# Optimization experiments

Measured on AMD Instinct MI355X. Metric: run time of the kernel, lower is better.

Reference implementation:

```python
import jax, jax.numpy as jnp
import numpy as np
from jax import lax

B, S, D, H, K, FF = 8, 1024, 512, 8, 3, 1024
BUCKETS, MAX_REL = 32, 128
DH = D // H
SPAN = BUCKETS  # att_span when position_buckets > 0


def setup_inputs() -> dict:
    key = jax.random.key(0)
    ks = jax.random.split(key, 12)
    n = lambda k, shp, s=0.02: jax.random.normal(k, shp, jnp.float32) * s
    return dict(
        x=jax.random.normal(ks[0], (B, S, D), jnp.float32),
        ln1_g=jnp.ones((D,), jnp.float32), ln1_b=jnp.zeros((D,), jnp.float32),
        dw_w=n(ks[1], (D, 1, K), 0.1), dw_b=jnp.zeros((D,), jnp.float32),
        pw_w=n(ks[2], (D, D)), pw_b=jnp.zeros((D,), jnp.float32),
        ln2_g=jnp.ones((D,), jnp.float32), ln2_b=jnp.zeros((D,), jnp.float32),
        q_w=n(ks[3], (D, D)), q_b=jnp.zeros((D,), jnp.float32),
        k_w=n(ks[4], (D, D)), k_b=jnp.zeros((D,), jnp.float32),
        v_w=n(ks[5], (D, D)), v_b=jnp.zeros((D,), jnp.float32),
        o_w=n(ks[6], (D, D)), o_b=jnp.zeros((D,), jnp.float32),
        rel_emb=n(ks[7], (2 * SPAN, D)),
        ln3_g=jnp.ones((D,), jnp.float32), ln3_b=jnp.zeros((D,), jnp.float32),
        w1=n(ks[8], (FF, D)), b1=jnp.zeros((FF,), jnp.float32),
        w2=n(ks[9], (D, FF)), b2=jnp.zeros((D,), jnp.float32),
    )


def _ln(x, g, b):
    m = x.mean(-1, keepdims=True)
    v = jnp.var(x, axis=-1, keepdims=True)
    return (x - m) * lax.rsqrt(v + 1e-5) * g + b


def _rel_bucket():
    # DeBERTa-v2 log-bucket relative positions, [S, S] int32
    ids = jnp.arange(S, dtype=jnp.int32)
    rel = ids[:, None] - ids[None, :]
    mid = BUCKETS // 2
    sign = jnp.sign(rel)
    abs_pos = jnp.where((rel < mid) & (rel > -mid), mid - 1, jnp.abs(rel)).astype(jnp.float32)
    log_pos = jnp.ceil(jnp.log(abs_pos / mid) / np.log((MAX_REL - 1) / mid) * (mid - 1)) + mid
    return jnp.where(abs_pos <= mid, rel, (log_pos * sign).astype(jnp.int32)).astype(jnp.int32)


def _attention(x, q_w, q_b, k_w, k_b, v_w, v_b, o_w, o_b, rel_emb):
    def heads(t):  # [B,S,D] -> [B,H,S,DH]
        return t.reshape(B, S, H, DH).transpose(0, 2, 1, 3)

    q = heads(x @ q_w.T + q_b)
    k = heads(x @ k_w.T + k_b)
    v = heads(x @ v_w.T + v_b)
    scale = 1.0 / np.sqrt(DH * 3)  # scale_factor = 1 + len(['c2p','p2c'])

    scores = jnp.einsum('bhid,bhjd->bhij', q, k) * scale  # content-to-content

    rel = _rel_bucket()  # [S,S]
    # shared att key: project rel embeddings with same q/k projections -> [H, 2*SPAN, DH]
    pos_k = (rel_emb @ k_w.T + k_b).reshape(2 * SPAN, H, DH).transpose(1, 0, 2)
    pos_q = (rel_emb @ q_w.T + q_b).reshape(2 * SPAN, H, DH).transpose(1, 0, 2)

    # content-to-position
    c2p = jnp.einsum('bhid,hjd->bhij', q, pos_k)  # [B,H,S,2*SPAN]
    c2p_idx = jnp.clip(rel + SPAN, 0, 2 * SPAN - 1)[None, None]  # [1,1,S,S]
    scores = scores + jnp.take_along_axis(c2p, c2p_idx, axis=-1) * scale

    # position-to-content
    p2c = jnp.einsum('bhid,hjd->bhij', k, pos_q)  # [B,H,S,2*SPAN]
    p2c_idx = jnp.clip(-rel + SPAN, 0, 2 * SPAN - 1)[None, None]
    scores = scores + jnp.take_along_axis(p2c, p2c_idx, axis=-1).swapaxes(-1, -2) * scale

    probs = jax.nn.softmax(scores, axis=-1)
    ctx = jnp.einsum('bhij,bhjd->bhid', probs, v).transpose(0, 2, 1, 3).reshape(B, S, D)
    return ctx @ o_w.T + o_b


def reference(x, ln1_g, ln1_b, dw_w, dw_b, pw_w, pw_b, ln2_g, ln2_b,
              q_w, q_b, k_w, k_b, v_w, v_b, o_w, o_b, rel_emb,
              ln3_g, ln3_b, w1, b1, w2, b2):
    # conv block (pre-norm)
    res = x
    xn = _ln(x, ln1_g, ln1_b)
    xc = xn.transpose(0, 2, 1)  # [B,D,S]
    dw = lax.conv_general_dilated(xc, dw_w, (1,), [(K // 2, K // 2)],
                                  dimension_numbers=('NCH', 'OIH', 'NCH'),
                                  feature_group_count=D) + dw_b[None, :, None]
    pw = jnp.einsum('od,bds->bos', pw_w, jax.nn.silu(dw)) + pw_b[None, :, None]
    x = res + pw.transpose(0, 2, 1)
    # attention block
    res = x
    x = res + _attention(_ln(x, ln2_g, ln2_b), q_w, q_b, k_w, k_b, v_w, v_b, o_w, o_b, rel_emb)
    # FFN block
    res = x
    xn = _ln(x, ln3_g, ln3_b)
    ff = jax.nn.silu(xn @ w1.T + b1) @ w2.T + b2
    return res + ff
```

## Files before the change

### kernel.cpp

```cpp
#include <hip/hip_runtime.h>
#include <hip/hip_bf16.h>
#include <math.h>


#define B_  8
#define S_  1024
#define D_  512
#define H_  8
#define DH_ 64
#define FF_ 1024
#define BS_ (B_*S_)
#define SCALE_ 0.07216878364f

typedef __attribute__((ext_vector_type(8))) short  short8;
typedef __attribute__((ext_vector_type(4))) short  short4v;
typedef __attribute__((ext_vector_type(4))) float  f32x4;
typedef __attribute__((ext_vector_type(4))) int    int4v;

static __device__ __forceinline__ float b2f(short u){
  union { int i; float f; } cv; cv.i = ((int)(unsigned short)u) << 16; return cv.f;
}
static __device__ __forceinline__ short f2b(float f){
  union { float f; unsigned u; } cv; cv.f = f;
  unsigned r = cv.u + 0x7FFFu + ((cv.u >> 16) & 1u);
  return (short)(r >> 16);
}
static __device__ __forceinline__ float silu_f(float x){
  return x / (1.f + __expf(-x));
}
static __device__ __forceinline__ f32x4 mfma16(short8 a, short8 b, f32x4 c){
  return __builtin_amdgcn_mfma_f32_16x16x32_bf16(a, b, c, 0, 0, 0);
}
static __device__ __forceinline__ void gl16(const void* g, void* l){
  __builtin_amdgcn_global_load_lds((const __attribute__((address_space(1))) void*)g,
                                   (__attribute__((address_space(3))) void*)l, 16, 0, 0);
}

struct F2B8 { const float* s[8]; short* d[8]; int n[8]; };
__global__ __launch_bounds__(256) void f2b8_kernel(F2B8 a){
  int seg = blockIdx.y;
  int i = (blockIdx.x*256 + threadIdx.x)*4;
  if (i >= a.n[seg]) return;
  float4 v = *(const float4*)(a.s[seg] + i);
  short4v o; o.x = f2b(v.x); o.y = f2b(v.y); o.z = f2b(v.z); o.w = f2b(v.w);
  *(short4v*)(a.d[seg] + i) = o;
}

__global__ __launch_bounds__(256) void tab_kernel(signed char* __restrict__ tab){
  int t = blockIdx.x*256 + threadIdx.x;
  if (t >= 2048) return;
  int d = t - 1023;
  int ad = d < 0 ? -d : d;
  int bkt;
  if (ad <= 16) bkt = d;
  else {
    const float inv_log = 15.f / logf(7.9375f);
    float lp = ceilf(logf((float)ad * (1.f/16.f)) * inv_log) + 16.f;
    int ilp = (int)lp;
    bkt = (d > 0) ? ilp : -ilp;
  }
  int idx = bkt + 32;
  idx = idx < 0 ? 0 : (idx > 63 ? 63 : idx);
  tab[t] = (signed char)idx;
}

__global__ __launch_bounds__(128) void ln_kernel(const float* __restrict__ x,
                                                 const float* __restrict__ g,
                                                 const float* __restrict__ bb,
                                                 short* __restrict__ out){
  int row = blockIdx.x;
  int tid = threadIdx.x;
  float4 v = ((const float4*)(x + (size_t)row*D_))[tid];
  float s  = v.x + v.y + v.z + v.w;
  float ss = v.x*v.x + v.y*v.y + v.z*v.z + v.w*v.w;
  #pragma unroll
  for (int off = 32; off; off >>= 1){ s += __shfl_down(s, off); ss += __shfl_down(ss, off); }
  __shared__ float red[4];
  if ((tid & 63) == 0){ red[tid>>6] = s; red[2 + (tid>>6)] = ss; }
  __syncthreads();
  float S  = red[0] + red[1];
  float SS = red[2] + red[3];
  float m   = S * (1.f/D_);
  float var = SS * (1.f/D_) - m*m;
  float rs  = rsqrtf(var + 1e-5f);
  float4 gv = ((const float4*)g)[tid];
  float4 bv = ((const float4*)bb)[tid];
  short4v o;
  o.x = f2b((v.x - m)*rs*gv.x + bv.x);
  o.y = f2b((v.y - m)*rs*gv.y + bv.y);
  o.z = f2b((v.z - m)*rs*gv.z + bv.z);
  o.w = f2b((v.w - m)*rs*gv.w + bv.w);
  *(short4v*)(out + (size_t)row*D_ + tid*4) = o;
}

__global__ __launch_bounds__(256) void dwconv_kernel(const short* __restrict__ xn,
                                                     const float* __restrict__ w,
                                                     const float* __restrict__ bias,
                                                     short* __restrict__ out){
  int idx = blockIdx.x*256 + threadIdx.x;
  int bs  = idx >> 6;
  int d8  = (idx & 63) << 3;
  int s   = bs & (S_-1);
  const short* base = xn + (size_t)bs*D_ + d8;
  short8 z = {};
  short8 xm = (s > 0)     ? *(const short8*)(base - D_) : z;
  short8 xc =               *(const short8*)(base);
  short8 xp = (s < S_-1)  ? *(const short8*)(base + D_) : z;
  short8 o;
  #pragma unroll
  for (int i = 0; i < 8; i++){
    int d = d8 + i;
    float acc = bias[d] + b2f(xm[i])*w[d*3+0] + b2f(xc[i])*w[d*3+1] + b2f(xp[i])*w[d*3+2];
    o[i] = f2b(silu_f(acc));
  }
  *(short8*)(out + (size_t)bs*D_ + d8) = o;
}

#define GEMM_GL_CORE(AP, WP, KK)                                               \
  __shared__ short a_lds[2][128*64];                                           \
  __shared__ short b_lds[2][64*64];                                            \
  int tid = threadIdx.x;                                                       \
  int w = tid >> 6, lane = tid & 63, quad = lane >> 4, l16 = lane & 15;        \
  int wm = (w >> 1) * 64, wn = (w & 1) * 32;                                   \
  int m0 = blockIdx.x * 128, n0 = blockIdx.y * 64;                             \
  int lr = lane >> 3, lc8 = ((lane & 7) ^ lr) * 8;                             \
  const short* asrc[4]; const short* bsrc[2];                                  \
  _Pragma("unroll")                                                            \
  for (int i = 0; i < 4; i++)                                                  \
    asrc[i] = AP + (size_t)(m0 + w*32 + i*8 + lr)*KK + lc8;                    \
  _Pragma("unroll")                                                            \
  for (int i = 0; i < 2; i++)                                                  \
    bsrc[i] = WP + (size_t)(n0 + w*16 + i*8 + lr)*KK + lc8;                    \
  f32x4 acc[4][2] = {};                                                        \
  int sx = l16 & 7;                                                            \
  _Pragma("unroll")                                                            \
  for (int i = 0; i < 4; i++) gl16(asrc[i], &a_lds[0][(w*32 + i*8)*64]);       \
  _Pragma("unroll")                                                            \
  for (int i = 0; i < 2; i++) gl16(bsrc[i], &b_lds[0][(w*16 + i*8)*64]);       \
  int cur = 0;                                                                 \
  for (int kk = 0; kk < KK; kk += 64){                                         \
    __syncthreads();                                                           \
    if (kk + 64 < KK){                                                         \
      _Pragma("unroll")                                                        \
      for (int i = 0; i < 4; i++)                                              \
        gl16(asrc[i] + kk + 64, &a_lds[cur^1][(w*32 + i*8)*64]);               \
      _Pragma("unroll")                                                        \
      for (int i = 0; i < 2; i++)                                              \
        gl16(bsrc[i] + kk + 64, &b_lds[cur^1][(w*16 + i*8)*64]);               \
    }                                                                          \
    _Pragma("unroll")                                                          \
    for (int ks = 0; ks < 2; ks++){                                            \
      short8 b0 = *(const short8*)&b_lds[cur][((wn      + l16)<<6) + (((ks*4+quad)^sx)<<3)]; \
      short8 b1 = *(const short8*)&b_lds[cur][((wn + 16 + l16)<<6) + (((ks*4+quad)^sx)<<3)]; \
      _Pragma("unroll")                                                        \
      for (int mt = 0; mt < 4; mt++){                                          \
        short8 a = *(const short8*)&a_lds[cur][((wm + mt*16 + l16)<<6) + (((ks*4+quad)^sx)<<3)]; \
        acc[mt][0] = mfma16(a, b0, acc[mt][0]);                                \
        acc[mt][1] = mfma16(a, b1, acc[mt][1]);                                \
      }                                                                        \
    }                                                                          \
    cur ^= 1;                                                                  \
  }

template<bool SILU, bool RES, bool OF32, bool OBF>
__global__ __launch_bounds__(256) void gemm_gl(const short* __restrict__ A,
                                               const short* __restrict__ W,
                                               const float* __restrict__ bias,
                                               const float* res,
                                               float* of32,
                                               short* __restrict__ obf,
                                               int M, int N, int K){
  GEMM_GL_CORE(A, W, K)
  #pragma unroll
  for (int mt = 0; mt < 4; mt++)
    #pragma unroll
    for (int nt = 0; nt < 2; nt++)
      #pragma unroll
      for (int r = 0; r < 4; r++){
        int row = m0 + wm + mt*16 + quad*4 + r;
        int col = n0 + wn + nt*16 + l16;
        float val = acc[mt][nt][r] + bias[col];
        if (SILU) val = silu_f(val);
        if (RES)  val += res[(size_t)row*N + col];
        if (OF32) of32[(size_t)row*N + col] = val;
        if (OBF)  obf[(size_t)row*N + col] = f2b(val);
      }
}

__global__ __launch_bounds__(256) void gemm_qkv(const short* __restrict__ A,
                                                const short* __restrict__ W,
                                                const float* __restrict__ qb,
                                                const float* __restrict__ kb,
                                                const float* __restrict__ vb,
                                                short* __restrict__ Qo,
                                                short* __restrict__ Ko,
                                                short* __restrict__ Vo,
                                                int M, int K){
  GEMM_GL_CORE(A, W, K)
  int colb = n0 + wn;
  int sel = colb >> 9;
  const float* bp = sel == 0 ? qb : (sel == 1 ? kb : vb);
  short* dp = sel == 0 ? Qo : (sel == 1 ? Ko : Vo);
  float mult = sel == 0 ? SCALE_ : 1.f;
  #pragma unroll
  for (int mt = 0; mt < 4; mt++)
    #pragma unroll
    for (int nt = 0; nt < 2; nt++)
      #pragma unroll
      for (int r = 0; r < 4; r++){
        int row = m0 + wm + mt*16 + quad*4 + r;
        int col = (colb + nt*16 + l16) & 511;
        float val = (acc[mt][nt][r] + bp[col]) * mult;
        dp[(size_t)row*D_ + col] = f2b(val);
      }
}

__global__ __launch_bounds__(256) void gemm_pos(const short* __restrict__ A,
                                                const short* __restrict__ W,
                                                const float* __restrict__ bias,
                                                short* __restrict__ obf,
                                                float mult, int N, int K){
  __shared__ short a_lds[64][72];
  __shared__ short b_lds[64][72];
  int tid = threadIdx.x;
  int w = tid >> 6, lane = tid & 63, quad = lane >> 4, l16 = lane & 15;
  int wm = (w >> 1) * 32, wn = (w & 1) * 32;
  int m0 = 0, n0 = blockIdx.x * 64;
  int r0 = tid >> 3, c0 = (tid & 7) * 8;
  int r1 = r0 + 32;
  f32x4 acc[2][2] = {};
  for (int kk = 0; kk < K; kk += 64){
    *(int4v*)&a_lds[r0][c0] = *(const int4v*)(A + (size_t)(m0+r0)*K + kk + c0);
    *(int4v*)&a_lds[r1][c0] = *(const int4v*)(A + (size_t)(m0+r1)*K + kk + c0);
    *(int4v*)&b_lds[r0][c0] = *(const int4v*)(W + (size_t)(n0+r0)*K + kk + c0);
    *(int4v*)&b_lds[r1][c0] = *(const int4v*)(W + (size_t)(n0+r1)*K + kk + c0);
    __syncthreads();
    #pragma unroll
    for (int ks = 0; ks < 2; ks++){
      short8 a0 = *(const short8*)&a_lds[wm      + l16][ks*32 + quad*8];
      short8 a1 = *(const short8*)&a_lds[wm + 16 + l16][ks*32 + quad*8];
      short8 b0 = *(const short8*)&b_lds[wn      + l16][ks*32 + quad*8];
      short8 b1 = *(const short8*)&b_lds[wn + 16 + l16][ks*32 + quad*8];
      acc[0][0] = mfma16(a0, b0, acc[0][0]);
      acc[0][1] = mfma16(a0, b1, acc[0][1]);
      acc[1][0] = mfma16(a1, b0, acc[1][0]);
      acc[1][1] = mfma16(a1, b1, acc[1][1]);
    }
    __syncthreads();
  }
  #pragma unroll
  for (int mt = 0; mt < 2; mt++)
    #pragma unroll
    for (int nt = 0; nt < 2; nt++)
      #pragma unroll
      for (int r = 0; r < 4; r++){
        int row = m0 + wm + mt*16 + quad*4 + r;
        int col = n0 + wn + nt*16 + l16;
        obf[(size_t)row*N + col] = f2b((acc[mt][nt][r] + bias[col]) * mult);
      }
}

__global__ __launch_bounds__(256) void posbias_kernel(const short* __restrict__ q,
                                                      const short* __restrict__ k,
                                                      const short* __restrict__ posk,
                                                      const short* __restrict__ posq,
                                                      short* __restrict__ c2p,
                                                      short* __restrict__ p2c,
                                                      short* __restrict__ pfar){
  int bsT = blockIdx.x;
  int h   = blockIdx.y;
  int tid = threadIdx.x, w = tid >> 6, lane = tid & 63, quad = lane >> 4, l16 = lane & 15;
  int row_a = bsT*64 + w*16 + l16;
  f32x4 accc[4] = {}, accp[4] = {};
  #pragma unroll
  for (int ks = 0; ks < 2; ks++){
    short8 aq = *(const short8*)(q + (size_t)row_a*D_ + h*DH_ + ks*32 + quad*8);
    short8 ak = *(const short8*)(k + (size_t)row_a*D_ + h*DH_ + ks*32 + quad*8);
    #pragma unroll
    for (int nt = 0; nt < 4; nt++){
      short8 bk = *(const short8*)(posk + (size_t)(nt*16+l16)*D_ + h*DH_ + ks*32 + quad*8);
      short8 bq = *(const short8*)(posq + (size_t)(nt*16+l16)*D_ + h*DH_ + ks*32 + quad*8);
      accc[nt] = mfma16(aq, bk, accc[nt]);
      accp[nt] = mfma16(ak, bq, accp[nt]);
    }
  }
  #pragma unroll
  for (int nt = 0; nt < 4; nt++)
    #pragma unroll
    for (int r = 0; r < 4; r++){
      int row = bsT*64 + w*16 + quad*4 + r;
      int col = h*DH_ + nt*16 + l16;
      short pv = f2b(accp[nt][r]);
      c2p[(size_t)row*D_ + col] = f2b(accc[nt][r]);
      p2c[(size_t)row*D_ + col] = pv;
      int cin = nt*16 + l16;
      if (cin == 0 || cin == 63){
        int b  = row >> 10, s = row & 1023;
        int bh = b*H_ + h;
        pfar[(size_t)bh*2048 + (cin ? 1024 : 0) + s] = pv;
      }
    }
}

__global__ __launch_bounds__(256) void vtrans_kernel(const short* __restrict__ v,
                                                     short* __restrict__ vt){
  __shared__ short t_lds[64][65];
  int st = blockIdx.x, h = blockIdx.y, b = blockIdx.z;
  int s0 = st*64;
  int tid = threadIdx.x;
  #pragma unroll
  for (int i = 0; i < 2; i++){
    int c = i*256 + tid;
    int s = c >> 3, d8 = (c & 7) * 8;
    short8 vv = *(const short8*)(v + (size_t)(b*S_ + s0 + s)*D_ + h*DH_ + d8);
    #pragma unroll
    for (int jj = 0; jj < 8; jj++) t_lds[d8+jj][s] = vv[jj];
  }
  __syncthreads();
  #pragma unroll
  for (int i = 0; i < 2; i++){
    int c = i*256 + tid;
    int d = c >> 3, s8 = (c & 7) * 8;
    short8 o;
    #pragma unroll
    for (int jj = 0; jj < 8; jj++) o[jj] = t_lds[d][s8+jj];
    *(short8*)(vt + ((size_t)(b*H_ + h)*DH_ + d)*S_ + s0 + s8) = o;
  }
}

#define PPS 68
__global__ __launch_bounds__(256, 4) void flash_kernel(const short* __restrict__ q,
                                                       const short* __restrict__ k,
                                                       const short* __restrict__ VT,
                                                       const short* __restrict__ c2p,
                                                       const short* __restrict__ p2c,
                                                       const short* __restrict__ PFAR,
                                                       const signed char* __restrict__ TAB,
                                                       short* __restrict__ ctx){
  __shared__ short k_lds[64*64];
  __shared__ short v_lds[64*64];
  __shared__ short c2p_lds[64][72];
  __shared__ short pp_lds[64][PPS];
  __shared__ signed char tab[2048];

  int bh = blockIdx.x, it = blockIdx.y;
  int b = bh >> 3, h = bh & 7;
  int i0 = it * 64;
  int tid = threadIdx.x, w = tid >> 6, lane = tid & 63, quad = lane >> 4, l16 = lane & 15;

  ((unsigned long long*)tab)[tid] = ((const unsigned long long*)TAB)[tid];
  #pragma unroll
  for (int i = 0; i < 2; i++){
    int c = i*256 + tid;
    int r = c >> 3, cc = (c & 7) * 8;
    *(int4v*)&c2p_lds[r][cc] = *(const int4v*)(c2p + (size_t)(b*S_ + i0 + r)*D_ + h*DH_ + cc);
  }
  short8 qf0, qf1;
  {
    size_t row = (size_t)(b*S_ + i0 + w*16 + l16);
    qf0 = *(const short8*)(q + row*D_ + h*DH_ +      quad*8);
    qf1 = *(const short8*)(q + row*D_ + h*DH_ + 32 + quad*8);
  }
  const short* Kbase  = k   + (size_t)(b*S_)*D_ + h*DH_;
  const short* VTbase = VT  + (size_t)(b*H_ + h)*DH_*S_;
  const short* Pbase  = p2c + (size_t)(b*S_)*D_ + h*DH_;
  const short* Fbase  = PFAR + (size_t)bh*2048;

  int lr = lane >> 3, lc8 = ((lane & 7) ^ lr) * 8;
  const short* ksrc[2]; const short* vsrc[2];
  #pragma unroll
  for (int i = 0; i < 2; i++){
    int rr = w*16 + i*8 + lr;
    ksrc[i] = Kbase  + (size_t)rr*D_ + lc8;
    vsrc[i] = VTbase + (size_t)rr*S_ + lc8;
  }
  int sx = l16 & 7;
  int st_r = tid >> 3, st_c = (tid & 7) * 8;

  __syncthreads();

  float cpos[4], cneg[4];
  #pragma unroll
  for (int r = 0; r < 4; r++){
    int iloc = w*16 + quad*4 + r;
    cpos[r] = b2f(c2p_lds[iloc][63]);
    cneg[r] = b2f(c2p_lds[iloc][0]);
  }
  f32x4 o_acc[4] = {};
  float lrow[4] = {};

  for (int jt = 0; jt < 16; jt++){
    int j0 = jt * 64;
    bool near = (jt >= it-2 && jt <= it+2);
    int4v ppv0, ppv1;
    if (near){
      ppv0 = *(const int4v*)(Pbase + (size_t)(j0 + st_r     )*D_ + st_c);
      ppv1 = *(const int4v*)(Pbase + (size_t)(j0 + st_r + 32)*D_ + st_c);
    }
    __syncthreads();
    #pragma unroll
    for (int i = 0; i < 2; i++){
      gl16(ksrc[i] + (size_t)j0*D_, &k_lds[(w*16 + i*8)*64]);
      gl16(vsrc[i] + j0,            &v_lds[(w*16 + i*8)*64]);
    }
    if (near){
      *(int4v*)&pp_lds[st_r     ][st_c] = ppv0;
      *(int4v*)&pp_lds[st_r + 32][st_c] = ppv1;
    }
    __syncthreads();

    f32x4 sfr[4];
    #pragma unroll
    for (int nt = 0; nt < 4; nt++){
      int rowb = (nt*16 + l16) << 6;
      f32x4 a = {};
      a = mfma16(qf0, *(const short8*)&k_lds[rowb + ((quad^sx)<<3)], a);
      a = mfma16(qf1, *(const short8*)&k_lds[rowb + (((quad+4)^sx)<<3)], a);
      sfr[nt] = a;
    }
    float pval[4][4];
    if (near){
      #pragma unroll
      for (int nt = 0; nt < 4; nt++){
        int jloc = nt*16 + l16;
        #pragma unroll
        for (int r = 0; r < 4; r++){
          int iloc = w*16 + quad*4 + r;
          int idx  = tab[(i0 + iloc) - (j0 + jloc) + 1023];
          float p = __expf(sfr[nt][r] + b2f(c2p_lds[iloc][idx]) + b2f(pp_lds[jloc][idx]));
          pval[nt][r] = p;
          lrow[r] += p;
        }
      }
      __syncthreads();
    } else {
      const float* cP = (jt < it) ? cpos : cneg;
      const short* fcol = Fbase + ((jt < it) ? 1024 : 0) + j0;
      #pragma unroll
      for (int nt = 0; nt < 4; nt++){
        float pv = b2f(fcol[nt*16 + l16]);
        #pragma unroll
        for (int r = 0; r < 4; r++){
          float p = __expf(sfr[nt][r] + cP[r] + pv);
          pval[nt][r] = p;
          lrow[r] += p;
        }
      }
    }

    #pragma unroll
    for (int nt = 0; nt < 4; nt++)
      #pragma unroll
      for (int r = 0; r < 4; r++)
        pp_lds[w*16 + quad*4 + r][nt*16 + l16] = f2b(pval[nt][r]);
    short8 pf0 = *(const short8*)&pp_lds[w*16 + l16][     quad*8];
    short8 pf1 = *(const short8*)&pp_lds[w*16 + l16][32 + quad*8];
    #pragma unroll
    for (int nt = 0; nt < 4; nt++){
      int rowb = (nt*16 + l16) << 6;
      o_acc[nt] = mfma16(pf0, *(const short8*)&v_lds[rowb + ((quad^sx)<<3)], o_acc[nt]);
      o_acc[nt] = mfma16(pf1, *(const short8*)&v_lds[rowb + (((quad+4)^sx)<<3)], o_acc[nt]);
    }
  }
  #pragma unroll
  for (int r = 0; r < 4; r++){
    #pragma unroll
    for (int off = 8; off; off >>= 1) lrow[r] += __shfl_xor(lrow[r], off);
  }
  #pragma unroll
  for (int nt = 0; nt < 4; nt++)
    #pragma unroll
    for (int r = 0; r < 4; r++){
      size_t row = (size_t)(b*S_ + i0 + w*16 + quad*4 + r);
      ctx[row*D_ + h*DH_ + nt*16 + l16] = f2b(o_acc[nt][r] / lrow[r]);
    }
}

static const size_t OFF_XN   = 0;
static const size_t OFF_Q    = 8388608;
static const size_t OFF_K    = 16777216;
static const size_t OFF_V    = 25165824;
static const size_t OFF_C2P  = 33554432;
static const size_t OFF_P2C  = 41943040;
static const size_t OFF_WPW  = 50331648;
static const size_t OFF_WQ   = 50855936;
static const size_t OFF_WK   = 51380224;
static const size_t OFF_WV   = 51904512;
static const size_t OFF_WO   = 52428800;
static const size_t OFF_W1   = 52953088;
static const size_t OFF_W2   = 54001664;
static const size_t OFF_REL  = 55050240;
static const size_t OFF_POSK = 55115776;
static const size_t OFF_POSQ = 55181312;
static const size_t OFF_TAB  = 55246848;
static const size_t OFF_PFAR = 55248896;

extern "C" void kernel_launch(void* const* d_in, const int* in_sizes, int n_in,
                              void* d_out, int out_size, void* d_ws, size_t ws_size,
                              hipStream_t stream){
  const float* x    = (const float*)d_in[0];
  const float* ln1g = (const float*)d_in[1];
  const float* ln1b = (const float*)d_in[2];
  const float* dww  = (const float*)d_in[3];
  const float* dwb  = (const float*)d_in[4];
  const float* pww  = (const float*)d_in[5];
  const float* pwb  = (const float*)d_in[6];
  const float* ln2g = (const float*)d_in[7];
  const float* ln2b = (const float*)d_in[8];
  const float* qw   = (const float*)d_in[9];
  const float* qb   = (const float*)d_in[10];
  const float* kw   = (const float*)d_in[11];
  const float* kb   = (const float*)d_in[12];
  const float* vw   = (const float*)d_in[13];
  const float* vb   = (const float*)d_in[14];
  const float* ow   = (const float*)d_in[15];
  const float* ob   = (const float*)d_in[16];
  const float* rel  = (const float*)d_in[17];
  const float* ln3g = (const float*)d_in[18];
  const float* ln3b = (const float*)d_in[19];
  const float* w1   = (const float*)d_in[20];
  const float* b1   = (const float*)d_in[21];
  const float* w2   = (const float*)d_in[22];
  const float* b2   = (const float*)d_in[23];
  float* out = (float*)d_out;
  char* ws = (char*)d_ws;

  short* XN   = (short*)(ws + OFF_XN);
  short* Q    = (short*)(ws + OFF_Q);
  short* Kb_  = (short*)(ws + OFF_K);
  short* V    = (short*)(ws + OFF_V);
  short* C2P  = (short*)(ws + OFF_C2P);
  short* P2C  = (short*)(ws + OFF_P2C);
  short* WPW  = (short*)(ws + OFF_WPW);
  short* WQ   = (short*)(ws + OFF_WQ);
  short* WK   = (short*)(ws + OFF_WK);
  short* WV   = (short*)(ws + OFF_WV);
  short* WO   = (short*)(ws + OFF_WO);
  short* W1B  = (short*)(ws + OFF_W1);
  short* W2B  = (short*)(ws + OFF_W2);
  short* RELB = (short*)(ws + OFF_REL);
  short* POSK = (short*)(ws + OFF_POSK);
  short* POSQ = (short*)(ws + OFF_POSQ);
  signed char* TAB = (signed char*)(ws + OFF_TAB);
  short* PFAR = (short*)(ws + OFF_PFAR);
  short* DWS  = C2P;
  short* VT   = XN;
  short* CTX  = V;
  short* FFH  = Q;

  F2B8 fa;
  fa.s[0]=pww; fa.d[0]=WPW; fa.n[0]=262144;
  fa.s[1]=qw;  fa.d[1]=WQ;  fa.n[1]=262144;
  fa.s[2]=kw;  fa.d[2]=WK;  fa.n[2]=262144;
  fa.s[3]=vw;  fa.d[3]=WV;  fa.n[3]=262144;
  fa.s[4]=ow;  fa.d[4]=WO;  fa.n[4]=262144;
  fa.s[5]=w1;  fa.d[5]=W1B; fa.n[5]=524288;
  fa.s[6]=w2;  fa.d[6]=W2B; fa.n[6]=524288;
  fa.s[7]=rel; fa.d[7]=RELB;fa.n[7]=32768;
  f2b8_kernel<<<dim3(512,8), 256, 0, stream>>>(fa);
  tab_kernel<<<8, 256, 0, stream>>>(TAB);

  ln_kernel<<<BS_, 128, 0, stream>>>(x, ln1g, ln1b, XN);
  dwconv_kernel<<<2048, 256, 0, stream>>>(XN, dww, dwb, DWS);
  gemm_gl<false,true,true,false><<<dim3(64,8), 256, 0, stream>>>(
      DWS, WPW, pwb, x, out, nullptr, BS_, 512, 512);

  ln_kernel<<<BS_, 128, 0, stream>>>(out, ln2g, ln2b, XN);
  gemm_qkv<<<dim3(64,24), 256, 0, stream>>>(
      XN, WQ, qb, kb, vb, Q, Kb_, V, BS_, 512);
  gemm_pos<<<8, 256, 0, stream>>>(RELB, WK, kb, POSK, 1.f,    512, 512);
  gemm_pos<<<8, 256, 0, stream>>>(RELB, WQ, qb, POSQ, SCALE_, 512, 512);
  posbias_kernel<<<dim3(128,8), 256, 0, stream>>>(Q, Kb_, POSK, POSQ, C2P, P2C, PFAR);
  vtrans_kernel<<<dim3(16,8,8), 256, 0, stream>>>(V, VT);
  flash_kernel<<<dim3(64,16), 256, 0, stream>>>(Q, Kb_, VT, C2P, P2C, PFAR, TAB, CTX);
  gemm_gl<false,true,true,false><<<dim3(64,8), 256, 0, stream>>>(
      CTX, WO, ob, out, out, nullptr, BS_, 512, 512);

  ln_kernel<<<BS_, 128, 0, stream>>>(out, ln3g, ln3b, XN);
  gemm_gl<true,false,false,true><<<dim3(64,16), 256, 0, stream>>>(
      XN, W1B, b1, nullptr, nullptr, FFH, BS_, 1024, 512);
  gemm_gl<false,true,true,false><<<dim3(64,8), 256, 0, stream>>>(
      FFH, W2B, b2, out, out, nullptr, BS_, 512, 1024);
}
```

Baseline: 323.2 us.

## Use 128x128 double-buffered GEMM tiles and transposed-score flash attention with K16 MFMA

Adds a GEMM core with 128x128 block tiles and double-buffered LDS prefetch, used for the QKV projection and the first FFN GEMM. This gives more reuse per tile and overlaps global loads with compute. The flash kernel is rewritten to compute transposed scores (K times Q), so the probabilities feed the 16x16x16 bf16 MFMA straight from registers. That removes the LDS round trip for P and the per-row shuffles. The larger tiles halve the grid size and raise register and LDS pressure.

```diff
diff --git a/kernel.cpp b/kernel.cpp
--- a/kernel.cpp
+++ b/kernel.cpp
@@ -16,6 +16,15 @@
 typedef __attribute__((ext_vector_type(4))) short  short4v;
 typedef __attribute__((ext_vector_type(4))) float  f32x4;
 typedef __attribute__((ext_vector_type(4))) int    int4v;
+
+#if __has_builtin(__builtin_amdgcn_mfma_f32_16x16x16bf16_1k)
+#define HAS_K16 1
+static __device__ __forceinline__ f32x4 mfma_k16(short4v a, short4v b, f32x4 c){
+  return __builtin_amdgcn_mfma_f32_16x16x16bf16_1k(a, b, c, 0, 0, 0);
+}
+#else
+#define HAS_K16 0
+#endif
 
 static __device__ __forceinline__ float b2f(short u){
   union { int i; float f; } cv; cv.i = ((int)(unsigned short)u) << 16; return cv.f;
@@ -187,16 +196,85 @@
       }
 }
 
-__global__ __launch_bounds__(256) void gemm_qkv(const short* __restrict__ A,
+#define GEMM_GL2_CORE(AP, WP, KK)                                              \
+  __shared__ short a_lds[2][128*64];                                           \
+  __shared__ short b_lds[2][128*64];                                           \
+  int tid = threadIdx.x;                                                       \
+  int w = tid >> 6, lane = tid & 63, quad = lane >> 4, l16 = lane & 15;        \
+  int wm = (w >> 1) * 64, wn = (w & 1) * 64;                                   \
+  int m0 = blockIdx.x * 128, n0 = blockIdx.y * 128;                            \
+  int lr = lane >> 3, lc8 = ((lane & 7) ^ lr) * 8;                             \
+  const short* asrc[4]; const short* bsrc[4];                                  \
+  _Pragma("unroll")                                                            \
+  for (int i = 0; i < 4; i++){                                                 \
+    asrc[i] = AP + (size_t)(m0 + w*32 + i*8 + lr)*KK + lc8;                    \
+    bsrc[i] = WP + (size_t)(n0 + w*32 + i*8 + lr)*KK + lc8;                    \
+  }                                                                            \
+  f32x4 acc[4][4] = {};                                                        \
+  int sx = l16 & 7;                                                            \
+  _Pragma("unroll")                                                            \
+  for (int i = 0; i < 4; i++){                                                 \
+    gl16(asrc[i], &a_lds[0][(w*32 + i*8)*64]);                                 \
+    gl16(bsrc[i], &b_lds[0][(w*32 + i*8)*64]);                                 \
+  }                                                                            \
+  int cur = 0;                                                                 \
+  for (int kk = 0; kk < KK; kk += 64){                                         \
+    __syncthreads();                                                           \
+    if (kk + 64 < KK){                                                         \
+      _Pragma("unroll")                                                        \
+      for (int i = 0; i < 4; i++){                                             \
+        gl16(asrc[i] + kk + 64, &a_lds[cur^1][(w*32 + i*8)*64]);               \
+        gl16(bsrc[i] + kk + 64, &b_lds[cur^1][(w*32 + i*8)*64]);               \
+      }                                                                        \
+    }                                                                          \
+    _Pragma("unroll")                                                          \
+    for (int ks = 0; ks < 2; ks++){                                            \
+      short8 bfr[4];                                                           \
+      _Pragma("unroll")                                                        \
+      for (int nt = 0; nt < 4; nt++)                                           \
+        bfr[nt] = *(const short8*)&b_lds[cur][((wn + nt*16 + l16)<<6) + (((ks*4+quad)^sx)<<3)]; \
+      _Pragma("unroll")                                                        \
+      for (int mt = 0; mt < 4; mt++){                                          \
+        short8 a = *(const short8*)&a_lds[cur][((wm + mt*16 + l16)<<6) + (((ks*4+quad)^sx)<<3)]; \
+        _Pragma("unroll")                                                      \
+        for (int nt = 0; nt < 4; nt++)                                         \
+          acc[mt][nt] = mfma16(a, bfr[nt], acc[mt][nt]);                       \
+      }                                                                        \
+    }                                                                          \
+    cur ^= 1;                                                                  \
+  }
+
+template<bool SILU, bool OBF>
+__global__ __launch_bounds__(256) void gemm_gl2(const short* __restrict__ A,
                                                 const short* __restrict__ W,
-                                                const float* __restrict__ qb,
-                                                const float* __restrict__ kb,
-                                                const float* __restrict__ vb,
-                                                short* __restrict__ Qo,
-                                                short* __restrict__ Ko,
-                                                short* __restrict__ Vo,
-                                                int M, int K){
-  GEMM_GL_CORE(A, W, K)
+                                                const float* __restrict__ bias,
+                                                short* __restrict__ obf,
+                                                int M, int N, int K){
+  GEMM_GL2_CORE(A, W, K)
+  #pragma unroll
+  for (int mt = 0; mt < 4; mt++)
+    #pragma unroll
+    for (int nt = 0; nt < 4; nt++)
+      #pragma unroll
+      for (int r = 0; r < 4; r++){
+        int row = m0 + wm + mt*16 + quad*4 + r;
+        int col = n0 + wn + nt*16 + l16;
+        float val = acc[mt][nt][r] + bias[col];
+        if (SILU) val = silu_f(val);
+        if (OBF)  obf[(size_t)row*N + col] = f2b(val);
+      }
+}
+
+__global__ __launch_bounds__(256) void gemm_qkv2(const short* __restrict__ A,
+                                                 const short* __restrict__ W,
+                                                 const float* __restrict__ qb,
+                                                 const float* __restrict__ kb,
+                                                 const float* __restrict__ vb,
+                                                 short* __restrict__ Qo,
+                                                 short* __restrict__ Ko,
+                                                 short* __restrict__ Vo,
+                                                 int M, int K){
+  GEMM_GL2_CORE(A, W, K)
   int colb = n0 + wn;
   int sel = colb >> 9;
   const float* bp = sel == 0 ? qb : (sel == 1 ? kb : vb);
@@ -205,7 +283,7 @@
   #pragma unroll
   for (int mt = 0; mt < 4; mt++)
     #pragma unroll
-    for (int nt = 0; nt < 2; nt++)
+    for (int nt = 0; nt < 4; nt++)
       #pragma unroll
       for (int r = 0; r < 4; r++){
         int row = m0 + wm + mt*16 + quad*4 + r;
@@ -328,6 +406,144 @@
   }
 }
 
+#if HAS_K16
+__global__ __launch_bounds__(256, 4) void flash_kernel(const short* __restrict__ q,
+                                                       const short* __restrict__ k,
+                                                       const short* __restrict__ VT,
+                                                       const short* __restrict__ c2p,
+                                                       const short* __restrict__ p2c,
+                                                       const short* __restrict__ PFAR,
+                                                       const signed char* __restrict__ TAB,
+                                                       short* __restrict__ ctx){
+  __shared__ short k_lds[64*64];
+  __shared__ short v_lds[64*64];
+  __shared__ short c2p_lds[64][72];
+  __shared__ short pp_lds[64][72];
+  __shared__ signed char tab[2048];
+
+  int bh = blockIdx.x, it = blockIdx.y;
+  int b = bh >> 3, h = bh & 7;
+  int i0 = it * 64;
+  int tid = threadIdx.x, w = tid >> 6, lane = tid & 63, quad = lane >> 4, l16 = lane & 15;
+
+  ((unsigned long long*)tab)[tid] = ((const unsigned long long*)TAB)[tid];
+  #pragma unroll
+  for (int i = 0; i < 2; i++){
+    int c = i*256 + tid;
+    int r = c >> 3, cc = (c & 7) * 8;
+    *(int4v*)&c2p_lds[r][cc] = *(const int4v*)(c2p + (size_t)(b*S_ + i0 + r)*D_ + h*DH_ + cc);
+  }
+  short8 qf0, qf1;
+  {
+    size_t row = (size_t)(b*S_ + i0 + w*16 + l16);
+    qf0 = *(const short8*)(q + row*D_ + h*DH_ +      quad*8);
+    qf1 = *(const short8*)(q + row*D_ + h*DH_ + 32 + quad*8);
+  }
+  const short* Kbase  = k   + (size_t)(b*S_)*D_ + h*DH_;
+  const short* VTbase = VT  + (size_t)(b*H_ + h)*DH_*S_;
+  const short* Pbase  = p2c + (size_t)(b*S_)*D_ + h*DH_;
+  const short* Fbase  = PFAR + (size_t)bh*2048;
+
+  int lr = lane >> 3, lc8 = ((lane & 7) ^ lr) * 8;
+  const short* ksrc[2]; const short* vsrc[2];
+  #pragma unroll
+  for (int i = 0; i < 2; i++){
+    int rr = w*16 + i*8 + lr;
+    ksrc[i] = Kbase  + (size_t)rr*D_ + lc8;
+    vsrc[i] = VTbase + (size_t)rr*S_ + lc8;
+  }
+  int sx = l16 & 7;
+  int st_r = tid >> 3, st_c = (tid & 7) * 8;
+
+  __syncthreads();
+  int myi = i0 + w*16 + l16;
+  float cpos = b2f(c2p_lds[w*16 + l16][63]);
+  float cneg = b2f(c2p_lds[w*16 + l16][0]);
+  f32x4 o_acc[4] = {};
+  float lrow = 0.f;
+
+  for (int jt = 0; jt < 16; jt++){
+    int j0 = jt * 64;
+    bool near = (jt >= it-2 && jt <= it+2);
+    int4v ppv0, ppv1;
+    if (near){
+      ppv0 = *(const int4v*)(Pbase + (size_t)(j0 + st_r     )*D_ + st_c);
+      ppv1 = *(const int4v*)(Pbase + (size_t)(j0 + st_r + 32)*D_ + st_c);
+    }
+    __syncthreads();
+    #pragma unroll
+    for (int i = 0; i < 2; i++){
+      gl16(ksrc[i] + (size_t)j0*D_, &k_lds[(w*16 + i*8)*64]);
+      gl16(vsrc[i] + j0,            &v_lds[(w*16 + i*8)*64]);
+    }
+    if (near){
+      *(int4v*)&pp_lds[st_r     ][st_c] = ppv0;
+      *(int4v*)&pp_lds[st_r + 32][st_c] = ppv1;
+    }
+    __syncthreads();
+
+    f32x4 sfr[4];
+    #pragma unroll
+    for (int js = 0; js < 4; js++){
+      int rowb = (js*16 + l16) << 6;
+      f32x4 a = {};
+      a = mfma16(*(const short8*)&k_lds[rowb + ((quad^sx)<<3)],     qf0, a);
+      a = mfma16(*(const short8*)&k_lds[rowb + (((quad+4)^sx)<<3)], qf1, a);
+      sfr[js] = a;
+    }
+    short4v pb[4];
+    if (near){
+      #pragma unroll
+      for (int js = 0; js < 4; js++){
+        #pragma unroll
+        for (int r = 0; r < 4; r++){
+          int j = j0 + js*16 + quad*4 + r;
+          int idx = tab[myi - j + 1023];
+          float p = __expf(sfr[js][r] + b2f(c2p_lds[w*16 + l16][idx])
+                                      + b2f(pp_lds[js*16 + quad*4 + r][idx]));
+          lrow += p;
+          pb[js][r] = f2b(p);
+        }
+      }
+    } else {
+      float cP = (jt < it) ? cpos : cneg;
+      const short* fcol = Fbase + ((jt < it) ? 1024 : 0) + j0;
+      #pragma unroll
+      for (int js = 0; js < 4; js++){
+        short4v pv4 = *(const short4v*)(fcol + js*16 + quad*4);
+        #pragma unroll
+        for (int r = 0; r < 4; r++){
+          float p = __expf(sfr[js][r] + cP + b2f(pv4[r]));
+          lrow += p;
+          pb[js][r] = f2b(p);
+        }
+      }
+    }
+    #pragma unroll
+    for (int js = 0; js < 4; js++){
+      #pragma unroll
+      for (int nt = 0; nt < 4; nt++){
+        int row = nt*16 + l16;
+        int chunk = (2*js + (quad >> 1)) ^ (row & 7);
+        const short* vp = &v_lds[(row << 6) + (chunk << 3) + ((quad & 1) << 2)];
+        o_acc[nt] = mfma_k16(pb[js], *(const short4v*)vp, o_acc[nt]);
+      }
+    }
+  }
+  lrow += __shfl_xor(lrow, 16);
+  lrow += __shfl_xor(lrow, 32);
+  float linv = 1.f / lrow;
+  #pragma unroll
+  for (int r = 0; r < 4; r++){
+    float li = __shfl(linv, quad*4 + r);
+    #pragma unroll
+    for (int nt = 0; nt < 4; nt++){
+      size_t row = (size_t)(b*S_ + i0 + w*16 + quad*4 + r);
+      ctx[row*D_ + h*DH_ + nt*16 + l16] = f2b(o_acc[nt][r] * li);
+    }
+  }
+}
+#else
 #define PPS 68
 __global__ __launch_bounds__(256, 4) void flash_kernel(const short* __restrict__ q,
                                                        const short* __restrict__ k,
@@ -342,12 +558,10 @@
   __shared__ short c2p_lds[64][72];
   __shared__ short pp_lds[64][PPS];
   __shared__ signed char tab[2048];
-
   int bh = blockIdx.x, it = blockIdx.y;
   int b = bh >> 3, h = bh & 7;
   int i0 = it * 64;
   int tid = threadIdx.x, w = tid >> 6, lane = tid & 63, quad = lane >> 4, l16 = lane & 15;
-
   ((unsigned long long*)tab)[tid] = ((const unsigned long long*)TAB)[tid];
   #pragma unroll
   for (int i = 0; i < 2; i++){
@@ -365,7 +579,6 @@
   const short* VTbase = VT  + (size_t)(b*H_ + h)*DH_*S_;
   const short* Pbase  = p2c + (size_t)(b*S_)*D_ + h*DH_;
   const short* Fbase  = PFAR + (size_t)bh*2048;
-
   int lr = lane >> 3, lc8 = ((lane & 7) ^ lr) * 8;
   const short* ksrc[2]; const short* vsrc[2];
   #pragma unroll
@@ -376,9 +589,7 @@
   }
   int sx = l16 & 7;
   int st_r = tid >> 3, st_c = (tid & 7) * 8;
-
   __syncthreads();
-
   float cpos[4], cneg[4];
   #pragma unroll
   for (int r = 0; r < 4; r++){
@@ -388,7 +599,6 @@
   }
   f32x4 o_acc[4] = {};
   float lrow[4] = {};
-
   for (int jt = 0; jt < 16; jt++){
     int j0 = jt * 64;
     bool near = (jt >= it-2 && jt <= it+2);
@@ -408,7 +618,6 @@
       *(int4v*)&pp_lds[st_r + 32][st_c] = ppv1;
     }
     __syncthreads();
-
     f32x4 sfr[4];
     #pragma unroll
     for (int nt = 0; nt < 4; nt++){
@@ -447,7 +656,6 @@
         }
       }
     }
-
     #pragma unroll
     for (int nt = 0; nt < 4; nt++)
       #pragma unroll
@@ -475,6 +683,7 @@
       ctx[row*D_ + h*DH_ + nt*16 + l16] = f2b(o_acc[nt][r] / lrow[r]);
     }
 }
+#endif
 
 static const size_t OFF_XN   = 0;
 static const size_t OFF_Q    = 8388608;
@@ -566,7 +775,7 @@
       DWS, WPW, pwb, x, out, nullptr, BS_, 512, 512);
 
   ln_kernel<<<BS_, 128, 0, stream>>>(out, ln2g, ln2b, XN);
-  gemm_qkv<<<dim3(64,24), 256, 0, stream>>>(
+  gemm_qkv2<<<dim3(64,12), 256, 0, stream>>>(
       XN, WQ, qb, kb, vb, Q, Kb_, V, BS_, 512);
   gemm_pos<<<8, 256, 0, stream>>>(RELB, WK, kb, POSK, 1.f,    512, 512);
   gemm_pos<<<8, 256, 0, stream>>>(RELB, WQ, qb, POSQ, SCALE_, 512, 512);
@@ -577,8 +786,8 @@
       CTX, WO, ob, out, out, nullptr, BS_, 512, 512);
 
   ln_kernel<<<BS_, 128, 0, stream>>>(out, ln3g, ln3b, XN);
-  gemm_gl<true,false,false,true><<<dim3(64,16), 256, 0, stream>>>(
-      XN, W1B, b1, nullptr, nullptr, FFH, BS_, 1024, 512);
+  gemm_gl2<true,true><<<dim3(64,8), 256, 0, stream>>>(
+      XN, W1B, b1, FFH, BS_, 1024, 512);
   gemm_gl<false,true,true,false><<<dim3(64,8), 256, 0, stream>>>(
       FFH, W2B, b2, out, out, nullptr, BS_, 512, 1024);
 }
```

New measurement: 321.6 us. No clear change (-0.5%).
